# Kernel optimization log

Hardware: AMD Instinct MI355X
Metric: run time of the kernel (lower is better)

Reference implementation:

```python
import jax, jax.numpy as jnp
import numpy as np

P = 128; D = 128; A = 128
NS = D * A            # sinogram nodes
NP = P * P            # pixel nodes
N = NS + NP           # total graph nodes
EPS = 1e-5
_PNAMES = ["af_w1","af_b1","af_p1","af_bn_g","af_bn_b","af_w2","af_b2","af_p2","af_w3","af_b3","af_p3","af_w4","af_b4","af_p4","af_w5","af_b5","af_p5","gcn_w","gcn_b","sr_w1","sr_b1","sr_p1","sr_w2","sr_b2","sr_p2","sr_w3","sr_b3","sr_p3"]


def _conv(x, w, b, pad):
    y = jax.lax.conv_general_dilated(x, w, (1, 1), [(pad, pad), (pad, pad)],
                                     dimension_numbers=("NCHW", "OIHW", "NCHW"))
    return y + b[None, :, None, None]


def _prelu(x, a):
    return jnp.where(x >= 0, x, a * x)


def _bn(x, g, b):
    # BatchNorm2d in training mode: biased batch stats over (N,H,W)
    m = x.mean(axis=(0, 2, 3), keepdims=True)
    v = x.var(axis=(0, 2, 3), keepdims=True)
    return (x - m) * jax.lax.rsqrt(v + EPS) * g[None, :, None, None] + b[None, :, None, None]


def _forward(sino, edge_index, edge_weight, p):
    # AndrewCNN sinogram filter: 1 -> 64 -> 64 -> 64 -> 64 -> 8, 7x7 convs
    h = _prelu(_conv(sino, p["af_w1"], p["af_b1"], 3), p["af_p1"])
    h = _bn(h, p["af_bn_g"], p["af_bn_b"])
    h = _prelu(_conv(h, p["af_w2"], p["af_b2"], 3), p["af_p2"])
    h = _prelu(_conv(h, p["af_w3"], p["af_b3"], 3), p["af_p3"])
    h = _prelu(_conv(h, p["af_w4"], p["af_b4"], 3), p["af_p4"])
    h = _prelu(_conv(h, p["af_w5"], p["af_b5"], 3), p["af_p5"])   # [B,8,D,A]
    B, F = h.shape[0], h.shape[1]
    # build_nodes_features (source_to_target): sino nodes first, zero pixel nodes
    flat_sino = h.transpose(0, 2, 3, 1).reshape(B, NS, F)
    x = jnp.concatenate([flat_sino, jnp.zeros((B, NP, F), h.dtype)], axis=1)  # [B,N,8]
    # GCNConv(8,10): lin -> gcn_norm with self loops -> scatter-add at targets -> +bias
    xl = x @ p["gcn_w"]                                            # [B,N,10]
    row, col = edge_index[0], edge_index[1]
    loop = jnp.arange(N)
    row2 = jnp.concatenate([row, loop])
    col2 = jnp.concatenate([col, loop])
    w2 = jnp.concatenate([edge_weight, jnp.ones((N,), edge_weight.dtype)])
    deg = jnp.zeros((N,), xl.dtype).at[col2].add(w2)
    dis = jnp.where(deg > 0, jax.lax.rsqrt(jnp.maximum(deg, EPS * 0 + 1e-30)), 0.0)
    norm = dis[row2] * w2 * dis[col2]                              # [E+N]
    msgs = xl[:, row2, :] * norm[None, :, None]                    # [B,E+N,10]
    agg = jnp.zeros_like(xl).at[:, col2, :].add(msgs) + p["gcn_b"]
    # keep pixel nodes, reshape to image grid
    img = agg[:, NS:, :].transpose(0, 2, 1).reshape(B, -1, P, P)   # [B,10,P,P]
    # SRNET: 10 -> 64 (9x9) -> 32 (1x1) -> 1 (5x5)
    o = _prelu(_conv(img, p["sr_w1"], p["sr_b1"], 4), p["sr_p1"])
    o = _prelu(_conv(o,   p["sr_w2"], p["sr_b2"], 0), p["sr_p2"])
    o = _prelu(_conv(o,   p["sr_w3"], p["sr_b3"], 2), p["sr_p3"])
    return o


def setup_inputs() -> dict:
    f = jnp.float32
    ks = jax.random.split(jax.random.key(0), 16)
    B, E = 4, 2097152
    def rn(k, shape, s):
        return jax.random.normal(k, shape, f) * s
    inp = {
        "sino": jax.random.normal(ks[0], (B, 1, D, A), f),
        "edge_index": jax.random.randint(ks[1], (2, E), 0, N),
        "edge_weight": jax.random.uniform(ks[2], (E,), f),
    }
    kw = jax.random.split(ks[3], 9)
    inp["af_w1"] = rn(kw[0], (64, 1, 7, 7), 0.2)
    inp["af_w2"] = rn(kw[1], (64, 64, 7, 7), 0.03)
    inp["af_w3"] = rn(kw[2], (64, 64, 7, 7), 0.03)
    inp["af_w4"] = rn(kw[3], (64, 64, 7, 7), 0.03)
    inp["af_w5"] = rn(kw[4], (8, 64, 7, 7), 0.03)
    inp["gcn_w"] = rn(kw[5], (8, 10), 0.3)
    inp["sr_w1"] = rn(kw[6], (64, 10, 9, 9), 0.05)
    inp["sr_w2"] = rn(kw[7], (32, 64, 1, 1), 0.18)
    inp["sr_w3"] = rn(kw[8], (1, 32, 5, 5), 0.05)
    for nm, c in [("af_b1", 64), ("af_b2", 64), ("af_b3", 64), ("af_b4", 64), ("af_b5", 8), ("sr_b1", 64), ("sr_b2", 32), ("sr_b3", 1)]:
        inp[nm] = jnp.zeros((c,), f)
    inp["gcn_b"] = jnp.zeros((10,), f)
    inp["af_bn_g"] = jnp.ones((64,), f)
    inp["af_bn_b"] = jnp.zeros((64,), f)
    for nm in ["af_p1", "af_p2", "af_p3", "af_p4", "af_p5", "sr_p1", "sr_p2", "sr_p3"]:
        inp[nm] = jnp.array(0.25, f)
    return inp


def reference(sino, edge_index, edge_weight, af_w1, af_b1, af_p1, af_bn_g, af_bn_b, af_w2, af_b2, af_p2, af_w3, af_b3, af_p3, af_w4, af_b4, af_p4, af_w5, af_b5, af_p5, gcn_w, gcn_b, sr_w1, sr_b1, sr_p1, sr_w2, sr_b2, sr_p2, sr_w3, sr_b3, sr_p3):
    p = dict(zip(_PNAMES, (af_w1, af_b1, af_p1, af_bn_g, af_bn_b, af_w2, af_b2, af_p2, af_w3, af_b3, af_p3, af_w4, af_b4, af_p4, af_w5, af_b5, af_p5, gcn_w, gcn_b, sr_w1, sr_b1, sr_p1, sr_w2, sr_b2, sr_p2, sr_w3, sr_b3, sr_p3)))
    return _forward(sino, edge_index, edge_weight, p)
```

## Files before the change

kernel.cpp:

```cpp
#include <hip/hip_runtime.h>

static constexpr int NS = 16384;

typedef __attribute__((ext_vector_type(8))) short bf16x8;
typedef __attribute__((ext_vector_type(4))) float f32x4;

__device__ inline unsigned short bf16_rne(float x) {
  unsigned u = __float_as_uint(x);
  unsigned r = u + 0x7FFF + ((u >> 16) & 1);
  return (unsigned short)(r >> 16);
}

__global__ void k_wtrans(const float* __restrict__ w, float* __restrict__ wT,
                         int CO, int CI_IN, int CI_OUT, int KS) {
  int i = blockIdx.x * 256 + threadIdx.x;
  int tot = KS * KS * CI_OUT * CO;
  if (i >= tot) return;
  int co = i % CO;
  int r = i / CO;
  int ci = r % CI_OUT;
  int t = r / CI_OUT;
  int ky = t / KS, kx = t % KS;
  float v = 0.f;
  if (ci < CI_IN) v = w[((co * CI_IN + ci) * KS + ky) * KS + kx];
  wT[i] = v;
}

__global__ void k_wpack(const float* __restrict__ w, unsigned short* __restrict__ wpk) {
  int i = blockIdx.x * 256 + threadIdx.x;
  if (i >= 49 * 64 * 64) return;
  int co = i & 63, r = i >> 6;
  int ci = r & 63, tap = r >> 6;
  float v = w[(co * 64 + ci) * 49 + tap];
  unsigned short hi = bf16_rne(v);
  float hif = __uint_as_float((unsigned)hi << 16);
  unsigned short lo = bf16_rne(v - hif);
  int ks = ci >> 5, k32 = ci & 31;
  int lane = ((k32 >> 3) << 4) | (co & 15);
  int j = ci & 7, nt = co >> 4;
  size_t base = ((size_t)(((tap * 2 + ks) * 4 + nt) * 2) * 64 + lane) * 8 + j;
  wpk[base] = hi;
  wpk[base + 512] = lo;
}

__global__ void k_wpack5(const float* __restrict__ w5,
                         unsigned short* __restrict__ wpk) {
  int i = blockIdx.x * 256 + threadIdx.x;
  if (i >= 196 * 512) return;
  int j = i & 7, l = (i >> 3) & 63, f = i >> 9;
  int sp = f & 1, r = f >> 1;
  int ks = r & 1, tap = r >> 1;
  int co = l & 15;
  int k32 = ((l >> 4) << 3) + j;
  int ci = ks * 32 + k32;
  float v = (co < 8) ? w5[(co * 64 + ci) * 49 + tap] : 0.f;
  unsigned short hi = bf16_rne(v);
  unsigned short outv;
  if (sp == 0) {
    outv = hi;
  } else {
    float hif = __uint_as_float((unsigned)hi << 16);
    outv = bf16_rne(v - hif);
  }
  wpk[i] = outv;
}

__global__ void k_wpacks(const float* __restrict__ sw1,
                         unsigned short* __restrict__ wpk) {
  int i = blockIdx.x * 256 + threadIdx.x;
  if (i >= 360 * 512) return;
  int j = i & 7, l = (i >> 3) & 63, f = i >> 9;
  int sp = f & 1, nt = (f >> 1) & 3;
  int r3 = f >> 3, p = r3 % 5, ky = r3 / 5;
  int co = nt * 16 + (l & 15);
  int k = ((l >> 4) << 3) + j;
  int kx = 2 * p + (k >> 4);
  int ci = k & 15;
  float v = (ci < 10 && kx < 9) ? sw1[((co * 10 + ci) * 9 + ky) * 9 + kx] : 0.f;
  unsigned short hi = bf16_rne(v);
  unsigned short outv;
  if (sp == 0) {
    outv = hi;
  } else {
    float hif = __uint_as_float((unsigned)hi << 16);
    outv = bf16_rne(v - hif);
  }
  wpk[i] = outv;
}

__global__ __launch_bounds__(128) void k_conv1(
    const float* __restrict__ sino, const float* __restrict__ wT1,
    const float* __restrict__ b1, const float* __restrict__ p1,
    float* __restrict__ out) {
  int b = blockIdx.x >> 7, y = blockIdx.x & 127, x = threadIdx.x;
  float acc[64];
#pragma unroll
  for (int i = 0; i < 64; ++i) acc[i] = 0.f;
#pragma unroll
  for (int ky = 0; ky < 7; ++ky) {
    int yy = y + ky - 3;
#pragma unroll
    for (int kx = 0; kx < 7; ++kx) {
      int xx = x + kx - 3;
      float v = (yy >= 0 && yy < 128 && xx >= 0 && xx < 128)
                    ? sino[(b * 128 + yy) * 128 + xx]
                    : 0.f;
      const float* wr = wT1 + (ky * 7 + kx) * 64;
#pragma unroll
      for (int co = 0; co < 64; ++co) acc[co] += v * wr[co];
    }
  }
  float a = p1[0];
  float* op = out + ((size_t)(b * 134 + y + 3) * 134 + x + 3) * 64;
#pragma unroll
  for (int co = 0; co < 64; ++co) {
    float v = acc[co] + b1[co];
    op[co] = v >= 0.f ? v : a * v;
  }
}

__global__ __launch_bounds__(256) void k_bnstats(const float* __restrict__ x1p,
                                                 double* __restrict__ bnsum) {
  int c = threadIdx.x & 63, sl = threadIdx.x >> 6;
  double s = 0.0, q = 0.0;
  int base = blockIdx.x * 512 + sl * 128;
  for (int i = 0; i < 128; ++i) {
    int p = base + i;
    int b = p >> 14, y = (p >> 7) & 127, x = p & 127;
    double v = (double)x1p[((size_t)(b * 134 + y + 3) * 134 + x + 3) * 64 + c];
    s += v;
    q += v * v;
  }
  __shared__ double red[2][4][64];
  red[0][sl][c] = s;
  red[1][sl][c] = q;
  __syncthreads();
  if (sl == 0) {
    s = red[0][0][c] + red[0][1][c] + red[0][2][c] + red[0][3][c];
    q = red[1][0][c] + red[1][1][c] + red[1][2][c] + red[1][3][c];
    atomicAdd(&bnsum[c], s);
    atomicAdd(&bnsum[64 + c], q);
  }
}

__global__ void k_bnfinal(const double* __restrict__ bnsum, float* __restrict__ bnsc,
                          const float* __restrict__ g, const float* __restrict__ bb) {
  int c = threadIdx.x;
  if (c >= 64) return;
  double m = bnsum[c] * (1.0 / 65536.0);
  double v = bnsum[64 + c] * (1.0 / 65536.0) - m * m;
  double sc = (double)g[c] * rsqrt(v + 1e-5);
  bnsc[c] = (float)sc;
  bnsc[64 + c] = (float)((double)bb[c] - m * sc);
}

__global__ __launch_bounds__(256) void k_bnapply(
    const float* __restrict__ x1p, const float* __restrict__ bnsc,
    unsigned short* __restrict__ oh, unsigned short* __restrict__ ol) {
  int i = blockIdx.x * 256 + threadIdx.x;
  if (i >= 4 * 128 * 128 * 16) return;
  int g = i & 15, p = i >> 4;
  int b = p >> 14, y = (p >> 7) & 127, x = p & 127;
  size_t base = ((size_t)(b * 134 + y + 3) * 134 + x + 3) * 64 + g * 4;
  float4 v = *(const float4*)(x1p + base);
  int c = g * 4;
  v.x = v.x * bnsc[c + 0] + bnsc[64 + c + 0];
  v.y = v.y * bnsc[c + 1] + bnsc[64 + c + 1];
  v.z = v.z * bnsc[c + 2] + bnsc[64 + c + 2];
  v.w = v.w * bnsc[c + 3] + bnsc[64 + c + 3];
  unsigned short h0 = bf16_rne(v.x), h1 = bf16_rne(v.y);
  unsigned short h2 = bf16_rne(v.z), h3 = bf16_rne(v.w);
  unsigned short l0 = bf16_rne(v.x - __uint_as_float((unsigned)h0 << 16));
  unsigned short l1 = bf16_rne(v.y - __uint_as_float((unsigned)h1 << 16));
  unsigned short l2 = bf16_rne(v.z - __uint_as_float((unsigned)h2 << 16));
  unsigned short l3 = bf16_rne(v.w - __uint_as_float((unsigned)h3 << 16));
  *(ushort4*)(oh + base) = make_ushort4(h0, h1, h2, h3);
  *(ushort4*)(ol + base) = make_ushort4(l0, l1, l2, l3);
}

__global__ __launch_bounds__(256) void k_convm(
    const unsigned short* __restrict__ inh, const unsigned short* __restrict__ inl,
    const unsigned short* __restrict__ wpk, const float* __restrict__ bias,
    const float* __restrict__ alpha, unsigned short* __restrict__ outh,
    unsigned short* __restrict__ outl) {
  int i0 = (int)((blockIdx.x & 7) * 64 + (blockIdx.x >> 3));
  int b = i0 >> 7, y = i0 & 127;
  int tid = threadIdx.x, l = tid & 63;
  int wv = tid >> 6;
  int pxb = (wv & 1) * 64;
  int coh = wv >> 1;
  int lg = l >> 4, lm = l & 15;

  __shared__ unsigned short hbuf[2][134 * 44];
  __shared__ unsigned short lbuf[2][134 * 44];

  f32x4 acc[4][2];
#pragma unroll
  for (int mt = 0; mt < 4; ++mt)
#pragma unroll
    for (int ntl = 0; ntl < 2; ++ntl) acc[mt][ntl] = (f32x4){0.f, 0.f, 0.f, 0.f};

  for (int ch = 0; ch < 64; ch += 32) {
    auto stage = [&](int ky, int s) {
      const unsigned short* gh = inh + ((size_t)(b * 134 + y + ky) * 134) * 64 + ch;
      const unsigned short* gl = inl + ((size_t)(b * 134 + y + ky) * 134) * 64 + ch;
      for (int i = tid; i < 134 * 4; i += 256) {
        int px = i >> 2, q = i & 3;
        bf16x8 vh = *(const bf16x8*)(gh + px * 64 + q * 8);
        bf16x8 vl = *(const bf16x8*)(gl + px * 64 + q * 8);
        *(bf16x8*)&hbuf[s][px * 44 + q * 8] = vh;
        *(bf16x8*)&lbuf[s][px * 44 + q * 8] = vl;
      }
    };
    stage(0, 0);
    __syncthreads();
    for (int ky = 0; ky < 7; ++ky) {
      if (ky < 6) stage(ky + 1, (ky + 1) & 1);
      int s = ky & 1;
#pragma unroll
      for (int kx = 0; kx < 7; ++kx) {
        int tap = ky * 7 + kx;
        const unsigned short* wt =
            wpk + (size_t)(tap * 2 + (ch >> 5)) * 8 * 512 + (size_t)l * 8;
        bf16x8 Bh[2], Bl[2];
#pragma unroll
        for (int ntl = 0; ntl < 2; ++ntl) {
          int nt = coh * 2 + ntl;
          Bh[ntl] = *(const bf16x8*)(wt + (nt * 2 + 0) * 512);
          Bl[ntl] = *(const bf16x8*)(wt + (nt * 2 + 1) * 512);
        }
#pragma unroll
        for (int mt = 0; mt < 4; ++mt) {
          int px = pxb + mt * 16 + lm + kx;
          bf16x8 Ah = *(const bf16x8*)&hbuf[s][px * 44 + lg * 8];
          bf16x8 Al = *(const bf16x8*)&lbuf[s][px * 44 + lg * 8];
#pragma unroll
          for (int ntl = 0; ntl < 2; ++ntl) {
            acc[mt][ntl] = __builtin_amdgcn_mfma_f32_16x16x32_bf16(Ah, Bh[ntl],
                                                                   acc[mt][ntl], 0, 0, 0);
            acc[mt][ntl] = __builtin_amdgcn_mfma_f32_16x16x32_bf16(Ah, Bl[ntl],
                                                                   acc[mt][ntl], 0, 0, 0);
            acc[mt][ntl] = __builtin_amdgcn_mfma_f32_16x16x32_bf16(Al, Bh[ntl],
                                                                   acc[mt][ntl], 0, 0, 0);
          }
        }
      }
      __syncthreads();
    }
  }
  float a = alpha[0];
#pragma unroll
  for (int mt = 0; mt < 4; ++mt)
#pragma unroll
    for (int ntl = 0; ntl < 2; ++ntl)
#pragma unroll
      for (int r = 0; r < 4; ++r) {
        int px = pxb + mt * 16 + lg * 4 + r;
        int co = coh * 32 + ntl * 16 + lm;
        float v = acc[mt][ntl][r] + bias[co];
        v = v >= 0.f ? v : a * v;
        unsigned short h = bf16_rne(v);
        unsigned short lo = bf16_rne(v - __uint_as_float((unsigned)h << 16));
        size_t idx = ((size_t)(b * 134 + y + 3) * 134 + px + 3) * 64 + co;
        outh[idx] = h;
        outl[idx] = lo;
      }
}

__global__ __launch_bounds__(256) void k_convm5(
    const unsigned short* __restrict__ inh, const unsigned short* __restrict__ inl,
    const unsigned short* __restrict__ wpk, const float* __restrict__ b5,
    const float* __restrict__ p5, const float* __restrict__ gw,
    float* __restrict__ xl) {
  int i0 = (int)((blockIdx.x & 7) * 64 + (blockIdx.x >> 3));
  int b = i0 >> 7, y = i0 & 127;
  int tid = threadIdx.x, l = tid & 63;
  int wv = tid >> 6;
  int pxb = wv * 32;
  int lg = l >> 4, lm = l & 15;

  __shared__ unsigned short hbuf[2][134 * 44];
  __shared__ unsigned short lbuf[2][134 * 44];
  __shared__ float feat[128][9];

  f32x4 acc[2];
  acc[0] = (f32x4){0.f, 0.f, 0.f, 0.f};
  acc[1] = (f32x4){0.f, 0.f, 0.f, 0.f};

  for (int ch = 0; ch < 64; ch += 32) {
    auto stage = [&](int ky, int s) {
      const unsigned short* gh = inh + ((size_t)(b * 134 + y + ky) * 134) * 64 + ch;
      const unsigned short* gl = inl + ((size_t)(b * 134 + y + ky) * 134) * 64 + ch;
      for (int i = tid; i < 134 * 4; i += 256) {
        int px = i >> 2, q = i & 3;
        bf16x8 vh = *(const bf16x8*)(gh + px * 64 + q * 8);
        bf16x8 vl = *(const bf16x8*)(gl + px * 64 + q * 8);
        *(bf16x8*)&hbuf[s][px * 44 + q * 8] = vh;
        *(bf16x8*)&lbuf[s][px * 44 + q * 8] = vl;
      }
    };
    stage(0, 0);
    __syncthreads();
    for (int ky = 0; ky < 7; ++ky) {
      if (ky < 6) stage(ky + 1, (ky + 1) & 1);
      int s = ky & 1;
#pragma unroll
      for (int kx = 0; kx < 7; ++kx) {
        int tap = ky * 7 + kx;
        const unsigned short* wt =
            wpk + (size_t)((tap * 2 + (ch >> 5)) * 2) * 512 + (size_t)l * 8;
        bf16x8 Bh = *(const bf16x8*)(wt);
        bf16x8 Bl = *(const bf16x8*)(wt + 512);
#pragma unroll
        for (int mt = 0; mt < 2; ++mt) {
          int px = pxb + mt * 16 + lm + kx;
          bf16x8 Ah = *(const bf16x8*)&hbuf[s][px * 44 + lg * 8];
          bf16x8 Al = *(const bf16x8*)&lbuf[s][px * 44 + lg * 8];
          acc[mt] = __builtin_amdgcn_mfma_f32_16x16x32_bf16(Ah, Bh, acc[mt], 0, 0, 0);
          acc[mt] = __builtin_amdgcn_mfma_f32_16x16x32_bf16(Ah, Bl, acc[mt], 0, 0, 0);
          acc[mt] = __builtin_amdgcn_mfma_f32_16x16x32_bf16(Al, Bh, acc[mt], 0, 0, 0);
        }
      }
      __syncthreads();
    }
  }
  float a = p5[0];
  if (lm < 8) {
#pragma unroll
    for (int mt = 0; mt < 2; ++mt)
#pragma unroll
      for (int r = 0; r < 4; ++r) {
        int px = pxb + mt * 16 + lg * 4 + r;
        float v = acc[mt][r] + b5[lm];
        feat[px][lm] = v >= 0.f ? v : a * v;
      }
  }
  __syncthreads();
  if (tid < 128) {
    int px = tid;
    float o[10];
#pragma unroll
    for (int f = 0; f < 10; ++f) o[f] = 0.f;
#pragma unroll
    for (int c = 0; c < 8; ++c) {
      float fv = feat[px][c];
#pragma unroll
      for (int f = 0; f < 10; ++f) o[f] += fv * gw[c * 10 + f];
    }
    float* op = xl + ((size_t)b * 16384 + y * 128 + px) * 10;
#pragma unroll
    for (int f = 0; f < 10; ++f) op[f] = o[f];
  }
}

__global__ __launch_bounds__(256) void k_convs(
    const float* __restrict__ imgp, const unsigned short* __restrict__ wpk,
    const float* __restrict__ bias, const float* __restrict__ alpha,
    float* __restrict__ out) {
  int i0 = (int)((blockIdx.x & 7) * 64 + (blockIdx.x >> 3));
  int b = i0 >> 7, y = i0 & 127;
  int tid = threadIdx.x, l = tid & 63;
  int wv = tid >> 6, wbase = wv * 32;
  int lg = l >> 4, lm = l & 15;

  __shared__ unsigned short hbuf[2][137 * 20];
  __shared__ unsigned short lbuf[2][137 * 20];

  f32x4 acc[2][4];
#pragma unroll
  for (int mt = 0; mt < 2; ++mt)
#pragma unroll
    for (int nt = 0; nt < 4; ++nt) acc[mt][nt] = (f32x4){0.f, 0.f, 0.f, 0.f};

  auto stage = [&](int ky, int s) {
    const float* gin = imgp + ((size_t)(b * 136 + y + ky) * 136) * 16;
    for (int i = tid; i < 137 * 4; i += 256) {
      int px = i >> 2, q = i & 3;
      float4 v = (px < 136) ? *(const float4*)(gin + px * 16 + q * 4)
                            : make_float4(0.f, 0.f, 0.f, 0.f);
      unsigned short h0 = bf16_rne(v.x), h1 = bf16_rne(v.y);
      unsigned short h2 = bf16_rne(v.z), h3 = bf16_rne(v.w);
      unsigned short l0 = bf16_rne(v.x - __uint_as_float((unsigned)h0 << 16));
      unsigned short l1 = bf16_rne(v.y - __uint_as_float((unsigned)h1 << 16));
      unsigned short l2 = bf16_rne(v.z - __uint_as_float((unsigned)h2 << 16));
      unsigned short l3 = bf16_rne(v.w - __uint_as_float((unsigned)h3 << 16));
      *(ushort4*)&hbuf[s][px * 20 + q * 4] = make_ushort4(h0, h1, h2, h3);
      *(ushort4*)&lbuf[s][px * 20 + q * 4] = make_ushort4(l0, l1, l2, l3);
    }
  };
  stage(0, 0);
  __syncthreads();
  for (int ky = 0; ky < 9; ++ky) {
    if (ky < 8) stage(ky + 1, (ky + 1) & 1);
    int s = ky & 1;
#pragma unroll
    for (int p = 0; p < 5; ++p) {
      const unsigned short* wt =
          wpk + ((size_t)(ky * 5 + p) * 8) * 512 + (size_t)l * 8;
      bf16x8 Bh[4], Bl[4];
#pragma unroll
      for (int nt = 0; nt < 4; ++nt) {
        Bh[nt] = *(const bf16x8*)(wt + (nt * 2 + 0) * 512);
        Bl[nt] = *(const bf16x8*)(wt + (nt * 2 + 1) * 512);
      }
#pragma unroll
      for (int mt = 0; mt < 2; ++mt) {
        int px = wbase + mt * 16 + lm + 2 * p + (lg >> 1);
        bf16x8 Ah = *(const bf16x8*)&hbuf[s][px * 20 + (lg & 1) * 8];
        bf16x8 Al = *(const bf16x8*)&lbuf[s][px * 20 + (lg & 1) * 8];
#pragma unroll
        for (int nt = 0; nt < 4; ++nt) {
          acc[mt][nt] =
              __builtin_amdgcn_mfma_f32_16x16x32_bf16(Ah, Bh[nt], acc[mt][nt], 0, 0, 0);
          acc[mt][nt] =
              __builtin_amdgcn_mfma_f32_16x16x32_bf16(Ah, Bl[nt], acc[mt][nt], 0, 0, 0);
          acc[mt][nt] =
              __builtin_amdgcn_mfma_f32_16x16x32_bf16(Al, Bh[nt], acc[mt][nt], 0, 0, 0);
        }
      }
    }
    __syncthreads();
  }
  float a = alpha[0];
#pragma unroll
  for (int mt = 0; mt < 2; ++mt)
#pragma unroll
    for (int nt = 0; nt < 4; ++nt)
#pragma unroll
      for (int r = 0; r < 4; ++r) {
        int px = wbase + mt * 16 + lg * 4 + r;
        int co = nt * 16 + lm;
        float v = acc[mt][nt][r] + bias[co];
        out[((size_t)(b * 128 + y) * 128 + px) * 64 + co] = v >= 0.f ? v : a * v;
      }
}

template <int CIN, int COUT, int KS, int IN_H, int IN_W, int OUT_H, int OUT_W,
          int OUT_OFF, int STR, int CH, int NSPLIT>
__global__ __launch_bounds__(64 * NSPLIT) void k_conv3(
    const float* __restrict__ in, const float* __restrict__ wT,
    const float* __restrict__ bias, const float* __restrict__ alpha,
    float* __restrict__ out) {
  constexpr int C = COUT / NSPLIT;
  int b = blockIdx.x >> 6, y0 = (blockIdx.x & 63) * 2;
  int l = threadIdx.x & 63;
  int cob = __builtin_amdgcn_readfirstlane((int)(threadIdx.x >> 6) * C);
  __shared__ float sbuf[2][IN_W * STR];
  float acc[4][C];
#pragma unroll
  for (int r = 0; r < 4; ++r)
#pragma unroll
    for (int i = 0; i < C; ++i) acc[r][i] = 0.f;

  for (int ch = 0; ch < CIN; ch += CH) {
    auto stage = [&](int k) {
      const float* gin = in + ((size_t)(b * IN_H + y0 + k) * IN_W) * CIN + ch;
      float* dst = sbuf[k & 1];
      constexpr int N4 = IN_W * CH / 4;
      for (int i = threadIdx.x; i < N4; i += 64 * NSPLIT) {
        int xx = i / (CH / 4), c4 = (i - xx * (CH / 4)) * 4;
        float4 v = *(const float4*)(gin + (size_t)xx * CIN + c4);
        *(float4*)(dst + xx * STR + c4) = v;
      }
    };
    stage(0);
    stage(1);
    __syncthreads();
    for (int ky = 0; ky < KS; ++ky) {
      const float* sA = sbuf[ky & 1];
      const float* sB = sbuf[(ky + 1) & 1];
      for (int kx = 0; kx < KS; ++kx) {
        const float* wt = wT + ((size_t)(ky * KS + kx) * CIN + ch) * COUT + cob;
        const float* a0p = sA + (l + kx) * STR;
        const float* a1p = sA + (l + 64 + kx) * STR;
        const float* b0p = sB + (l + kx) * STR;
        const float* b1p = sB + (l + 64 + kx) * STR;
#pragma unroll
        for (int ci = 0; ci < CH; ci += 4) {
          float4 a0 = *(const float4*)(a0p + ci);
          float4 a1 = *(const float4*)(a1p + ci);
          float4 b0 = *(const float4*)(b0p + ci);
          float4 b1 = *(const float4*)(b1p + ci);
#pragma unroll
          for (int c = 0; c < 4; ++c) {
            const float* wr = wt + (size_t)(ci + c) * COUT;
            float va0 = ((const float*)&a0)[c], va1 = ((const float*)&a1)[c];
            float vb0 = ((const float*)&b0)[c], vb1 = ((const float*)&b1)[c];
#pragma unroll
            for (int co = 0; co < C; ++co) {
              float w = wr[co];
              acc[0][co] += va0 * w;
              acc[1][co] += va1 * w;
              acc[2][co] += vb0 * w;
              acc[3][co] += vb1 * w;
            }
          }
        }
      }
      __syncthreads();
      if (ky < KS - 1) {
        stage(ky + 2);
        __syncthreads();
      }
    }
  }
  float a = alpha[0];
#pragma unroll
  for (int r = 0; r < 2; ++r) {
    float* rowp =
        out + (((size_t)(b * OUT_H + y0 + r + OUT_OFF)) * OUT_W + OUT_OFF) * COUT + cob;
#pragma unroll
    for (int p = 0; p < 2; ++p) {
      float* op = rowp + (size_t)(l + p * 64) * COUT;
#pragma unroll
      for (int co = 0; co < C; ++co) {
        float v = acc[r * 2 + p][co] + bias[cob + co];
        op[co] = v >= 0.f ? v : a * v;
      }
    }
  }
}

template <int CIN, int COUT, int KS, int IN_H, int IN_W, int OUT_H, int OUT_W,
          int OUT_OFF, int STR, int NSPLIT>
__global__ __launch_bounds__(64 * NSPLIT) void k_conv2(
    const float* __restrict__ in, const float* __restrict__ wT,
    const float* __restrict__ bias, const float* __restrict__ alpha,
    float* __restrict__ out) {
  constexpr int C = COUT / NSPLIT;
  int b = blockIdx.x >> 7, y = blockIdx.x & 127;
  int l = threadIdx.x & 63;
  int cob = __builtin_amdgcn_readfirstlane((int)(threadIdx.x >> 6) * C);
  __shared__ float srow[IN_W * STR];
  float acc0[C], acc1[C];
#pragma unroll
  for (int i = 0; i < C; ++i) acc0[i] = acc1[i] = 0.f;

  for (int ky = 0; ky < KS; ++ky) {
    __syncthreads();
    const float* gin = in + (size_t)(b * IN_H + y + ky) * IN_W * CIN;
    constexpr int N4 = IN_W * CIN / 4;
    for (int i = threadIdx.x; i < N4; i += 64 * NSPLIT) {
      float4 v = *(const float4*)(gin + (size_t)i * 4);
      int xx = (i * 4) / CIN, cc = (i * 4) % CIN;
      *(float4*)(srow + xx * STR + cc) = v;
    }
    __syncthreads();
    for (int kx = 0; kx < KS; ++kx) {
      const float* wt = wT + ((size_t)(ky * KS + kx) * CIN) * COUT + cob;
      const float* s0 = srow + (l + kx) * STR;
      const float* s1 = srow + (l + 64 + kx) * STR;
      for (int ci = 0; ci < CIN; ci += 4) {
        float4 a0 = *(const float4*)(s0 + ci);
        float4 a1 = *(const float4*)(s1 + ci);
#pragma unroll
        for (int c = 0; c < 4; ++c) {
          float v0 = ((const float*)&a0)[c];
          float v1 = ((const float*)&a1)[c];
          const float* wr = wt + (size_t)(ci + c) * COUT;
#pragma unroll
          for (int co = 0; co < C; ++co) {
            float w = wr[co];
            acc0[co] += v0 * w;
            acc1[co] += v1 * w;
          }
        }
      }
    }
  }
  float a = alpha[0];
  float* rowp = out + ((size_t)(b * OUT_H + y + OUT_OFF) * OUT_W + OUT_OFF) * COUT + cob;
  float* op0 = rowp + (size_t)l * COUT;
  float* op1 = rowp + (size_t)(l + 64) * COUT;
#pragma unroll
  for (int co = 0; co < C; ++co) {
    float bi = bias[cob + co];
    float v0 = acc0[co] + bi;
    float v1 = acc1[co] + bi;
    op0[co] = v0 >= 0.f ? v0 : a * v0;
    op1[co] = v1 >= 0.f ? v1 : a * v1;
  }
}

template <int HALF>
__global__ __launch_bounds__(1024) void k_degp(
    const int* __restrict__ ei, const float* __restrict__ ew,
    float* __restrict__ pdeg, int* __restrict__ cnt, int* __restrict__ rank, int E) {
  __shared__ float degl[16384];
  for (int i = threadIdx.x; i < 16384; i += 1024) degl[i] = 0.f;
  __syncthreads();
  int chunk = (E + gridDim.x - 1) / gridDim.x;
  int base = blockIdx.x * chunk;
  int end = min(E, base + chunk);
  for (int e = base + (int)threadIdx.x; e < end; e += 1024) {
    int col = ei[E + e];
    float w = ew[e];
    if ((col >> 14) == HALF) atomicAdd(&degl[col & 16383], w);
    if (HALF == 1) {
      int row = ei[e];
      if (row < NS && col >= NS) rank[e] = atomicAdd(&cnt[col - NS], 1);
    }
  }
  __syncthreads();
  float* pd = pdeg + (size_t)blockIdx.x * 16384;
  for (int i = threadIdx.x; i < 16384; i += 1024) pd[i] = degl[i];
}

__global__ void k_dis2(const float* __restrict__ pdegA, const float* __restrict__ pdegB,
                       float* __restrict__ dis, int nb) {
  int n = blockIdx.x * 256 + threadIdx.x;
  if (n >= 2 * NS) return;
  const float* p = (n < NS ? pdegA : pdegB) + (n & 16383);
  float s = 1.0f;
  for (int b = 0; b < nb; ++b) s += p[(size_t)b * 16384];
  dis[n] = rsqrtf(s);
}

__global__ __launch_bounds__(1024) void k_scan(const int* __restrict__ cnt,
                                               int* __restrict__ ptr) {
  __shared__ int ps[1024];
  int tid = threadIdx.x;
  int base = tid * 16;
  int v[16];
  int s = 0;
#pragma unroll
  for (int k = 0; k < 16; ++k) {
    v[k] = s;
    s += cnt[base + k];
  }
  ps[tid] = s;
  __syncthreads();
  for (int off = 1; off < 1024; off <<= 1) {
    int t = (tid >= off) ? ps[tid - off] : 0;
    __syncthreads();
    ps[tid] += t;
    __syncthreads();
  }
  int chunkoff = (tid == 0) ? 0 : ps[tid - 1];
#pragma unroll
  for (int k = 0; k < 16; ++k) ptr[base + k] = chunkoff + v[k];
  if (tid == 1023) ptr[16384] = ps[1023];
}

__global__ void k_bucket2(const int* __restrict__ ei, const float* __restrict__ ew,
                          const float* __restrict__ dis, const int* __restrict__ ptr,
                          const int* __restrict__ rank, int* __restrict__ erow,
                          float* __restrict__ enrm, int E) {
  int e = blockIdx.x * 256 + threadIdx.x;
  if (e >= E) return;
  int row = ei[e], col = ei[E + e];
  if (row >= NS || col < NS) return;
  int cp = col - NS;
  int pos = ptr[cp] + rank[e];
  erow[pos] = row;
  enrm[pos] = dis[row] * ew[e] * dis[col];
}

__global__ __launch_bounds__(256) void k_gather(
    const int* __restrict__ ptr, const int* __restrict__ erow,
    const float* __restrict__ enrm, const float* __restrict__ xl,
    const float* __restrict__ gb, float* __restrict__ imgp) {
  int cp = blockIdx.x * 4 + (threadIdx.x >> 6);
  int l = threadIdx.x & 63;
  int b = l >> 4, f = l & 15;
  bool act = f < 10;
  float acc = 0.f;
  int s = ptr[cp], e1 = ptr[cp + 1];
  for (int e = s; e < e1; ++e) {
    int row = erow[e];
    float nrm = enrm[e];
    if (act) acc += xl[((size_t)b * 16384 + row) * 10 + f] * nrm;
  }
  if (act) {
    int y = cp >> 7, x = cp & 127;
    imgp[((size_t)(b * 136 + y + 4) * 136 + x + 4) * 16 + f] = acc + gb[f];
  }
}

extern "C" void kernel_launch(void* const* d_in, const int* in_sizes, int n_in,
                              void* d_out, int out_size, void* d_ws, size_t ws_size,
                              hipStream_t stream) {
  const float* sino = (const float*)d_in[0];
  const int* ei = (const int*)d_in[1];
  const float* ew = (const float*)d_in[2];
  const float* w1 = (const float*)d_in[3];
  const float* w2 = (const float*)d_in[4];
  const float* w3 = (const float*)d_in[5];
  const float* w4 = (const float*)d_in[6];
  const float* w5 = (const float*)d_in[7];
  const float* gw = (const float*)d_in[8];
  const float* sw1 = (const float*)d_in[9];
  const float* sw2 = (const float*)d_in[10];
  const float* sw3 = (const float*)d_in[11];
  const float* b1 = (const float*)d_in[12];
  const float* b2 = (const float*)d_in[13];
  const float* b3 = (const float*)d_in[14];
  const float* b4 = (const float*)d_in[15];
  const float* b5 = (const float*)d_in[16];
  const float* sb1 = (const float*)d_in[17];
  const float* sb2 = (const float*)d_in[18];
  const float* sb3 = (const float*)d_in[19];
  const float* gb = (const float*)d_in[20];
  const float* bng = (const float*)d_in[21];
  const float* bnb = (const float*)d_in[22];
  const float* p1 = (const float*)d_in[23];
  const float* p2 = (const float*)d_in[24];
  const float* p3 = (const float*)d_in[25];
  const float* p4 = (const float*)d_in[26];
  const float* p5 = (const float*)d_in[27];
  const float* sp1 = (const float*)d_in[28];
  const float* sp2 = (const float*)d_in[29];
  const float* sp3 = (const float*)d_in[30];
  const int E = in_sizes[2];

  char* ws = (char*)d_ws;
  size_t off = 0;
  auto alloc = [&](size_t bytes) {
    char* p = ws + off;
    off += (bytes + 255) & ~(size_t)255;
    return p;
  };
  const size_t PL = (size_t)4 * 134 * 134 * 64;
  float* x1p = (float*)alloc(PL * 4);
  unsigned short* xh1 = (unsigned short*)alloc(PL * 2);
  unsigned short* xl1 = (unsigned short*)alloc(PL * 2);
  unsigned short* xh2 = (unsigned short*)alloc(PL * 2);
  unsigned short* xl2 = (unsigned short*)alloc(PL * 2);
  unsigned short* wpk2 = (unsigned short*)alloc(401408 * 2);
  unsigned short* wpk3 = (unsigned short*)alloc(401408 * 2);
  unsigned short* wpk4 = (unsigned short*)alloc(401408 * 2);
  unsigned short* wpk5 = (unsigned short*)alloc(100352 * 2);
  unsigned short* wpks1 = (unsigned short*)alloc(184320 * 2);
  float* wt1 = (float*)alloc(3136 * 4);
  float* wts2 = (float*)alloc(2048 * 4);
  float* wts3 = (float*)alloc(800 * 4);
  double* bnsum = (double*)alloc(128 * 8);
  float* bnsc = (float*)alloc(128 * 4);
  float* xl = (float*)alloc((size_t)4 * 16384 * 10 * 4);
  float* pdegA = (float*)alloc((size_t)64 * 16384 * 4);
  float* pdegB = (float*)alloc((size_t)64 * 16384 * 4);
  float* dis = (float*)alloc(32768 * 4);
  int* cnt = (int*)alloc(16384 * 4);
  int* ptr = (int*)alloc(16385 * 4);
  int* rank = (int*)alloc((size_t)E * 4);
  int* erow = (int*)alloc((size_t)E * 4);
  float* enrm = (float*)alloc((size_t)E * 4);
  float* imgp = (float*)alloc((size_t)4 * 136 * 136 * 16 * 4);
  float* s1 = (float*)alloc((size_t)4 * 128 * 128 * 64 * 4);
  float* s2p = (float*)alloc((size_t)4 * 132 * 132 * 32 * 4);

  hipMemsetAsync(xh1, 0, PL * 2, stream);
  hipMemsetAsync(xl1, 0, PL * 2, stream);
  hipMemsetAsync(xh2, 0, PL * 2, stream);
  hipMemsetAsync(xl2, 0, PL * 2, stream);
  hipMemsetAsync(bnsum, 0, 128 * 8, stream);
  hipMemsetAsync(cnt, 0, 16384 * 4, stream);
  hipMemsetAsync(imgp, 0, (size_t)4 * 136 * 136 * 16 * 4, stream);
  hipMemsetAsync(s2p, 0, (size_t)4 * 132 * 132 * 32 * 4, stream);

  k_wpack<<<784, 256, 0, stream>>>(w2, wpk2);
  k_wpack<<<784, 256, 0, stream>>>(w3, wpk3);
  k_wpack<<<784, 256, 0, stream>>>(w4, wpk4);
  k_wpack5<<<392, 256, 0, stream>>>(w5, wpk5);
  k_wpacks<<<720, 256, 0, stream>>>(sw1, wpks1);
  k_wtrans<<<13, 256, 0, stream>>>(w1, wt1, 64, 1, 1, 7);
  k_wtrans<<<8, 256, 0, stream>>>(sw2, wts2, 32, 64, 64, 1);
  k_wtrans<<<4, 256, 0, stream>>>(sw3, wts3, 1, 32, 32, 5);

  k_conv1<<<512, 128, 0, stream>>>(sino, wt1, b1, p1, x1p);
  k_bnstats<<<128, 256, 0, stream>>>(x1p, bnsum);
  k_bnfinal<<<1, 64, 0, stream>>>(bnsum, bnsc, bng, bnb);
  k_bnapply<<<4096, 256, 0, stream>>>(x1p, bnsc, xh1, xl1);

  k_convm<<<512, 256, 0, stream>>>(xh1, xl1, wpk2, b2, p2, xh2, xl2);
  k_convm<<<512, 256, 0, stream>>>(xh2, xl2, wpk3, b3, p3, xh1, xl1);
  k_convm<<<512, 256, 0, stream>>>(xh1, xl1, wpk4, b4, p4, xh2, xl2);
  k_convm5<<<512, 256, 0, stream>>>(xh2, xl2, wpk5, b5, p5, gw, xl);

  k_degp<0><<<64, 1024, 0, stream>>>(ei, ew, pdegA, cnt, rank, E);
  k_degp<1><<<64, 1024, 0, stream>>>(ei, ew, pdegB, cnt, rank, E);
  k_dis2<<<128, 256, 0, stream>>>(pdegA, pdegB, dis, 64);
  k_scan<<<1, 1024, 0, stream>>>(cnt, ptr);
  k_bucket2<<<(E + 255) / 256, 256, 0, stream>>>(ei, ew, dis, ptr, rank, erow, enrm, E);
  k_gather<<<4096, 256, 0, stream>>>(ptr, erow, enrm, xl, gb, imgp);

  k_convs<<<512, 256, 0, stream>>>(imgp, wpks1, sb1, sp1, s1);
  k_conv3<64, 32, 1, 128, 128, 132, 132, 2, 36, 32, 8>
      <<<256, 512, 0, stream>>>(s1, wts2, sb2, sp2, s2p);
  k_conv2<32, 1, 5, 132, 132, 128, 128, 0, 36, 1>
      <<<512, 64, 0, stream>>>(s2p, wts3, sb3, sp3, (float*)d_out);
}
```

Baseline: 632.7 us.

## Pre-split gather output to bf16 hi/lo and replace SR 1x1/5x5 convs with per-pixel kernels

The gather kernel now writes its padded image directly as bf16 high/low planes, so the first SR conv only copies them into shared memory instead of converting floats on every staged row. The 1x1 SR conv (64->32) and the final 5x5 conv (32->1) replace the LDS-tiled templated kernels with simple one-thread-per-pixel kernels, which spread the work over more threads. The per-pixel kernels read weights through uniform global loads and reread neighbouring inputs from cache rather than from shared memory.

```diff
diff --git a/kernel.cpp b/kernel.cpp
--- a/kernel.cpp
+++ b/kernel.cpp
@@ -354,9 +354,9 @@
 }
 
 __global__ __launch_bounds__(256) void k_convs(
-    const float* __restrict__ imgp, const unsigned short* __restrict__ wpk,
-    const float* __restrict__ bias, const float* __restrict__ alpha,
-    float* __restrict__ out) {
+    const unsigned short* __restrict__ imgph, const unsigned short* __restrict__ imgpl,
+    const unsigned short* __restrict__ wpk, const float* __restrict__ bias,
+    const float* __restrict__ alpha, float* __restrict__ out) {
   int i0 = (int)((blockIdx.x & 7) * 64 + (blockIdx.x >> 3));
   int b = i0 >> 7, y = i0 & 127;
   int tid = threadIdx.x, l = tid & 63;
@@ -372,20 +372,16 @@
 #pragma unroll
     for (int nt = 0; nt < 4; ++nt) acc[mt][nt] = (f32x4){0.f, 0.f, 0.f, 0.f};
 
+  bf16x8 zz = (bf16x8){0, 0, 0, 0, 0, 0, 0, 0};
   auto stage = [&](int ky, int s) {
-    const float* gin = imgp + ((size_t)(b * 136 + y + ky) * 136) * 16;
-    for (int i = tid; i < 137 * 4; i += 256) {
-      int px = i >> 2, q = i & 3;
-      float4 v = (px < 136) ? *(const float4*)(gin + px * 16 + q * 4)
-                            : make_float4(0.f, 0.f, 0.f, 0.f);
-      unsigned short h0 = bf16_rne(v.x), h1 = bf16_rne(v.y);
-      unsigned short h2 = bf16_rne(v.z), h3 = bf16_rne(v.w);
-      unsigned short l0 = bf16_rne(v.x - __uint_as_float((unsigned)h0 << 16));
-      unsigned short l1 = bf16_rne(v.y - __uint_as_float((unsigned)h1 << 16));
-      unsigned short l2 = bf16_rne(v.z - __uint_as_float((unsigned)h2 << 16));
-      unsigned short l3 = bf16_rne(v.w - __uint_as_float((unsigned)h3 << 16));
-      *(ushort4*)&hbuf[s][px * 20 + q * 4] = make_ushort4(h0, h1, h2, h3);
-      *(ushort4*)&lbuf[s][px * 20 + q * 4] = make_ushort4(l0, l1, l2, l3);
+    const unsigned short* gh = imgph + ((size_t)(b * 136 + y + ky) * 136) * 16;
+    const unsigned short* gl = imgpl + ((size_t)(b * 136 + y + ky) * 136) * 16;
+    for (int i = tid; i < 137 * 2; i += 256) {
+      int px = i >> 1, q = i & 1;
+      bf16x8 vh = (px < 136) ? *(const bf16x8*)(gh + px * 16 + q * 8) : zz;
+      bf16x8 vl = (px < 136) ? *(const bf16x8*)(gl + px * 16 + q * 8) : zz;
+      *(bf16x8*)&hbuf[s][px * 20 + q * 8] = vh;
+      *(bf16x8*)&lbuf[s][px * 20 + q * 8] = vl;
     }
   };
   stage(0, 0);
@@ -435,151 +431,61 @@
       }
 }
 
-template <int CIN, int COUT, int KS, int IN_H, int IN_W, int OUT_H, int OUT_W,
-          int OUT_OFF, int STR, int CH, int NSPLIT>
-__global__ __launch_bounds__(64 * NSPLIT) void k_conv3(
-    const float* __restrict__ in, const float* __restrict__ wT,
+__global__ __launch_bounds__(256) void k_sr2(
+    const float* __restrict__ s1, const float* __restrict__ wt,
+    const float* __restrict__ bias, const float* __restrict__ alpha,
+    float* __restrict__ s2p) {
+  int i = blockIdx.x * 256 + threadIdx.x;
+  if (i >= 4 * 16384) return;
+  int b = i >> 14, n = i & 16383, y = n >> 7, x = n & 127;
+  const float* ip = s1 + (size_t)i * 64;
+  float acc[32];
+#pragma unroll
+  for (int co = 0; co < 32; ++co) acc[co] = 0.f;
+#pragma unroll
+  for (int ci = 0; ci < 64; ci += 4) {
+    float4 v = *(const float4*)(ip + ci);
+#pragma unroll
+    for (int c = 0; c < 4; ++c) {
+      float vv = ((const float*)&v)[c];
+      const float* wr = wt + (ci + c) * 32;
+#pragma unroll
+      for (int co = 0; co < 32; ++co) acc[co] += vv * wr[co];
+    }
+  }
+  float a = alpha[0];
+  float* op = s2p + ((size_t)(b * 132 + y + 2) * 132 + x + 2) * 32;
+#pragma unroll
+  for (int co = 0; co < 32; ++co) {
+    float v = acc[co] + bias[co];
+    op[co] = v >= 0.f ? v : a * v;
+  }
+}
+
+__global__ __launch_bounds__(256) void k_sr3(
+    const float* __restrict__ s2p, const float* __restrict__ wt,
     const float* __restrict__ bias, const float* __restrict__ alpha,
     float* __restrict__ out) {
-  constexpr int C = COUT / NSPLIT;
-  int b = blockIdx.x >> 6, y0 = (blockIdx.x & 63) * 2;
-  int l = threadIdx.x & 63;
-  int cob = __builtin_amdgcn_readfirstlane((int)(threadIdx.x >> 6) * C);
-  __shared__ float sbuf[2][IN_W * STR];
-  float acc[4][C];
-#pragma unroll
-  for (int r = 0; r < 4; ++r)
-#pragma unroll
-    for (int i = 0; i < C; ++i) acc[r][i] = 0.f;
-
-  for (int ch = 0; ch < CIN; ch += CH) {
-    auto stage = [&](int k) {
-      const float* gin = in + ((size_t)(b * IN_H + y0 + k) * IN_W) * CIN + ch;
-      float* dst = sbuf[k & 1];
-      constexpr int N4 = IN_W * CH / 4;
-      for (int i = threadIdx.x; i < N4; i += 64 * NSPLIT) {
-        int xx = i / (CH / 4), c4 = (i - xx * (CH / 4)) * 4;
-        float4 v = *(const float4*)(gin + (size_t)xx * CIN + c4);
-        *(float4*)(dst + xx * STR + c4) = v;
-      }
-    };
-    stage(0);
-    stage(1);
-    __syncthreads();
-    for (int ky = 0; ky < KS; ++ky) {
-      const float* sA = sbuf[ky & 1];
-      const float* sB = sbuf[(ky + 1) & 1];
-      for (int kx = 0; kx < KS; ++kx) {
-        const float* wt = wT + ((size_t)(ky * KS + kx) * CIN + ch) * COUT + cob;
-        const float* a0p = sA + (l + kx) * STR;
-        const float* a1p = sA + (l + 64 + kx) * STR;
-        const float* b0p = sB + (l + kx) * STR;
-        const float* b1p = sB + (l + 64 + kx) * STR;
-#pragma unroll
-        for (int ci = 0; ci < CH; ci += 4) {
-          float4 a0 = *(const float4*)(a0p + ci);
-          float4 a1 = *(const float4*)(a1p + ci);
-          float4 b0 = *(const float4*)(b0p + ci);
-          float4 b1 = *(const float4*)(b1p + ci);
-#pragma unroll
-          for (int c = 0; c < 4; ++c) {
-            const float* wr = wt + (size_t)(ci + c) * COUT;
-            float va0 = ((const float*)&a0)[c], va1 = ((const float*)&a1)[c];
-            float vb0 = ((const float*)&b0)[c], vb1 = ((const float*)&b1)[c];
-#pragma unroll
-            for (int co = 0; co < C; ++co) {
-              float w = wr[co];
-              acc[0][co] += va0 * w;
-              acc[1][co] += va1 * w;
-              acc[2][co] += vb0 * w;
-              acc[3][co] += vb1 * w;
-            }
-          }
-        }
-      }
-      __syncthreads();
-      if (ky < KS - 1) {
-        stage(ky + 2);
-        __syncthreads();
+  int i = blockIdx.x * 256 + threadIdx.x;
+  if (i >= 4 * 16384) return;
+  int b = i >> 14, n = i & 16383, y = n >> 7, x = n & 127;
+  float acc = 0.f;
+#pragma unroll
+  for (int ky = 0; ky < 5; ++ky) {
+#pragma unroll
+    for (int kx = 0; kx < 5; ++kx) {
+      const float* wr = wt + (ky * 5 + kx) * 32;
+      const float* ip = s2p + ((size_t)(b * 132 + y + ky) * 132 + x + kx) * 32;
+#pragma unroll
+      for (int ci = 0; ci < 32; ci += 4) {
+        float4 v = *(const float4*)(ip + ci);
+        acc += v.x * wr[ci] + v.y * wr[ci + 1] + v.z * wr[ci + 2] + v.w * wr[ci + 3];
       }
     }
   }
   float a = alpha[0];
-#pragma unroll
-  for (int r = 0; r < 2; ++r) {
-    float* rowp =
-        out + (((size_t)(b * OUT_H + y0 + r + OUT_OFF)) * OUT_W + OUT_OFF) * COUT + cob;
-#pragma unroll
-    for (int p = 0; p < 2; ++p) {
-      float* op = rowp + (size_t)(l + p * 64) * COUT;
-#pragma unroll
-      for (int co = 0; co < C; ++co) {
-        float v = acc[r * 2 + p][co] + bias[cob + co];
-        op[co] = v >= 0.f ? v : a * v;
-      }
-    }
-  }
-}
-
-template <int CIN, int COUT, int KS, int IN_H, int IN_W, int OUT_H, int OUT_W,
-          int OUT_OFF, int STR, int NSPLIT>
-__global__ __launch_bounds__(64 * NSPLIT) void k_conv2(
-    const float* __restrict__ in, const float* __restrict__ wT,
-    const float* __restrict__ bias, const float* __restrict__ alpha,
-    float* __restrict__ out) {
-  constexpr int C = COUT / NSPLIT;
-  int b = blockIdx.x >> 7, y = blockIdx.x & 127;
-  int l = threadIdx.x & 63;
-  int cob = __builtin_amdgcn_readfirstlane((int)(threadIdx.x >> 6) * C);
-  __shared__ float srow[IN_W * STR];
-  float acc0[C], acc1[C];
-#pragma unroll
-  for (int i = 0; i < C; ++i) acc0[i] = acc1[i] = 0.f;
-
-  for (int ky = 0; ky < KS; ++ky) {
-    __syncthreads();
-    const float* gin = in + (size_t)(b * IN_H + y + ky) * IN_W * CIN;
-    constexpr int N4 = IN_W * CIN / 4;
-    for (int i = threadIdx.x; i < N4; i += 64 * NSPLIT) {
-      float4 v = *(const float4*)(gin + (size_t)i * 4);
-      int xx = (i * 4) / CIN, cc = (i * 4) % CIN;
-      *(float4*)(srow + xx * STR + cc) = v;
-    }
-    __syncthreads();
-    for (int kx = 0; kx < KS; ++kx) {
-      const float* wt = wT + ((size_t)(ky * KS + kx) * CIN) * COUT + cob;
-      const float* s0 = srow + (l + kx) * STR;
-      const float* s1 = srow + (l + 64 + kx) * STR;
-      for (int ci = 0; ci < CIN; ci += 4) {
-        float4 a0 = *(const float4*)(s0 + ci);
-        float4 a1 = *(const float4*)(s1 + ci);
-#pragma unroll
-        for (int c = 0; c < 4; ++c) {
-          float v0 = ((const float*)&a0)[c];
-          float v1 = ((const float*)&a1)[c];
-          const float* wr = wt + (size_t)(ci + c) * COUT;
-#pragma unroll
-          for (int co = 0; co < C; ++co) {
-            float w = wr[co];
-            acc0[co] += v0 * w;
-            acc1[co] += v1 * w;
-          }
-        }
-      }
-    }
-  }
-  float a = alpha[0];
-  float* rowp = out + ((size_t)(b * OUT_H + y + OUT_OFF) * OUT_W + OUT_OFF) * COUT + cob;
-  float* op0 = rowp + (size_t)l * COUT;
-  float* op1 = rowp + (size_t)(l + 64) * COUT;
-#pragma unroll
-  for (int co = 0; co < C; ++co) {
-    float bi = bias[cob + co];
-    float v0 = acc0[co] + bi;
-    float v1 = acc1[co] + bi;
-    op0[co] = v0 >= 0.f ? v0 : a * v0;
-    op1[co] = v1 >= 0.f ? v1 : a * v1;
-  }
+  float v = acc + bias[0];
+  out[i] = v >= 0.f ? v : a * v;
 }
 
 template <int HALF>
@@ -659,7 +565,8 @@
 __global__ __launch_bounds__(256) void k_gather(
     const int* __restrict__ ptr, const int* __restrict__ erow,
     const float* __restrict__ enrm, const float* __restrict__ xl,
-    const float* __restrict__ gb, float* __restrict__ imgp) {
+    const float* __restrict__ gb, unsigned short* __restrict__ imgph,
+    unsigned short* __restrict__ imgpl) {
   int cp = blockIdx.x * 4 + (threadIdx.x >> 6);
   int l = threadIdx.x & 63;
   int b = l >> 4, f = l & 15;
@@ -673,7 +580,12 @@
   }
   if (act) {
     int y = cp >> 7, x = cp & 127;
-    imgp[((size_t)(b * 136 + y + 4) * 136 + x + 4) * 16 + f] = acc + gb[f];
+    float v = acc + gb[f];
+    unsigned short h = bf16_rne(v);
+    unsigned short lo = bf16_rne(v - __uint_as_float((unsigned)h << 16));
+    size_t idx = ((size_t)(b * 136 + y + 4) * 136 + x + 4) * 16 + f;
+    imgph[idx] = h;
+    imgpl[idx] = lo;
   }
 }
 
@@ -721,6 +633,7 @@
     return p;
   };
   const size_t PL = (size_t)4 * 134 * 134 * 64;
+  const size_t IPL = (size_t)4 * 136 * 136 * 16;
   float* x1p = (float*)alloc(PL * 4);
   unsigned short* xh1 = (unsigned short*)alloc(PL * 2);
   unsigned short* xl1 = (unsigned short*)alloc(PL * 2);
@@ -745,7 +658,8 @@
   int* rank = (int*)alloc((size_t)E * 4);
   int* erow = (int*)alloc((size_t)E * 4);
   float* enrm = (float*)alloc((size_t)E * 4);
-  float* imgp = (float*)alloc((size_t)4 * 136 * 136 * 16 * 4);
+  unsigned short* imgph = (unsigned short*)alloc(IPL * 2);
+  unsigned short* imgpl = (unsigned short*)alloc(IPL * 2);
   float* s1 = (float*)alloc((size_t)4 * 128 * 128 * 64 * 4);
   float* s2p = (float*)alloc((size_t)4 * 132 * 132 * 32 * 4);
 
@@ -755,7 +669,8 @@
   hipMemsetAsync(xl2, 0, PL * 2, stream);
   hipMemsetAsync(bnsum, 0, 128 * 8, stream);
   hipMemsetAsync(cnt, 0, 16384 * 4, stream);
-  hipMemsetAsync(imgp, 0, (size_t)4 * 136 * 136 * 16 * 4, stream);
+  hipMemsetAsync(imgph, 0, IPL * 2, stream);
+  hipMemsetAsync(imgpl, 0, IPL * 2, stream);
   hipMemsetAsync(s2p, 0, (size_t)4 * 132 * 132 * 32 * 4, stream);
 
   k_wpack<<<784, 256, 0, stream>>>(w2, wpk2);
@@ -782,11 +697,9 @@
   k_dis2<<<128, 256, 0, stream>>>(pdegA, pdegB, dis, 64);
   k_scan<<<1, 1024, 0, stream>>>(cnt, ptr);
   k_bucket2<<<(E + 255) / 256, 256, 0, stream>>>(ei, ew, dis, ptr, rank, erow, enrm, E);
-  k_gather<<<4096, 256, 0, stream>>>(ptr, erow, enrm, xl, gb, imgp);
-
-  k_convs<<<512, 256, 0, stream>>>(imgp, wpks1, sb1, sp1, s1);
-  k_conv3<64, 32, 1, 128, 128, 132, 132, 2, 36, 32, 8>
-      <<<256, 512, 0, stream>>>(s1, wts2, sb2, sp2, s2p);
-  k_conv2<32, 1, 5, 132, 132, 128, 128, 0, 36, 1>
-      <<<512, 64, 0, stream>>>(s2p, wts3, sb3, sp3, (float*)d_out);
-}
+  k_gather<<<4096, 256, 0, stream>>>(ptr, erow, enrm, xl, gb, imgph, imgpl);
+
+  k_convs<<<512, 256, 0, stream>>>(imgph, imgpl, wpks1, sb1, sp1, s1);
+  k_sr2<<<256, 256, 0, stream>>>(s1, wts2, sb2, sp2, s2p);
+  k_sr3<<<256, 256, 0, stream>>>(s2p, wts3, sb3, sp3, (float*)d_out);
+}
```

New measurement: 619.8 us, median of 2. 1.02x faster.
